# Optimization experiments

Hardware: AMD Instinct MI355X
Metric: run time of the kernel (lower is better)

## Reference

```python
import jax, jax.numpy as jnp
import numpy as np

N = 100000
E = 1600000
C = 64          # hidden_channels
F_IN = 3
F_OUT = 3
N_MP = 2        # message-passing layers


def _lin(k, fan_in, fan_out):
    kw, kb = jax.random.split(k)
    bound = 1.0 / np.sqrt(fan_in)
    W = jax.random.uniform(kw, (fan_in, fan_out), jnp.float32, -bound, bound)
    b = jax.random.uniform(kb, (fan_out,), jnp.float32, -bound, bound)
    return W, b


def setup_inputs() -> dict:
    key = jax.random.key(0)
    ks = jax.random.split(key, 32)
    x = jax.random.normal(ks[0], (N, F_IN), jnp.float32)
    pos = jax.random.normal(ks[1], (N, 3), jnp.float32)
    edge_index = jax.random.randint(ks[2], (2, E), 0, N, jnp.int64)

    enc_W0, enc_b0 = _lin(ks[3], F_IN, C)
    enc_W1, enc_b1 = _lin(ks[4], C, C)
    dec_W0, dec_b0 = _lin(ks[5], C, C)
    dec_W1, dec_b1 = _lin(ks[6], C, F_OUT)

    # stacked params for the N_MP message-passing layers
    eW0, eb0, eW1, eb1 = [], [], [], []
    nW0, nb0, nW1, nb1 = [], [], [], []
    for i in range(N_MP):
        W, b = _lin(ks[7 + 4 * i], 3 * C + 3, C); eW0.append(W); eb0.append(b)
        W, b = _lin(ks[8 + 4 * i], C, C);         eW1.append(W); eb1.append(b)
        W, b = _lin(ks[9 + 4 * i], 2 * C, C);     nW0.append(W); nb0.append(b)
        W, b = _lin(ks[10 + 4 * i], C, C);        nW1.append(W); nb1.append(b)
    stack = lambda xs: jnp.stack(xs, axis=0)
    return {
        "x": x, "pos": pos, "edge_index": edge_index,
        "enc_W0": enc_W0, "enc_b0": enc_b0, "enc_W1": enc_W1, "enc_b1": enc_b1,
        "dec_W0": dec_W0, "dec_b0": dec_b0, "dec_W1": dec_W1, "dec_b1": dec_b1,
        "mp_eW0": stack(eW0), "mp_eb0": stack(eb0),
        "mp_eW1": stack(eW1), "mp_eb1": stack(eb1),
        "mp_nW0": stack(nW0), "mp_nb0": stack(nb0),
        "mp_nW1": stack(nW1), "mp_nb1": stack(nb1),
    }


def reference(x, pos, edge_index,
              enc_W0, enc_b0, enc_W1, enc_b1,
              dec_W0, dec_b0, dec_W1, dec_b1,
              mp_eW0, mp_eb0, mp_eW1, mp_eb1,
              mp_nW0, mp_nb0, mp_nW1, mp_nb1):
    act = jax.nn.elu
    src, dst = edge_index[0], edge_index[1]

    # node encoder (2-layer MLP, activation between layers only)
    h = act(x @ enc_W0 + enc_b0)
    h = h @ enc_W1 + enc_b1

    pos_diff = pos[src] - pos[dst]  # [E, 3], constant across MP layers

    for i in range(N_MP):
        x_nei = h[src]               # [E, C]
        x_own = h[dst]               # [E, C]
        ea = jnp.concatenate([x_nei, x_own, x_nei - x_own, pos_diff], axis=1)
        ea = act(ea @ mp_eW0[i] + mp_eb0[i])
        ea = ea @ mp_eW1[i] + mp_eb1[i]
        # EdgeAggregation(aggr='add'): scatter-add edge features to target nodes
        agg = jax.ops.segment_sum(ea, dst, num_segments=N)  # [N, C]
        u = jnp.concatenate([h, agg], axis=1)                # [N, 2C]
        u = act(u @ mp_nW0[i] + mp_nb0[i])
        u = u @ mp_nW1[i] + mp_nb1[i]
        h = h + u  # residual

    # node decoder
    out = act(h @ dec_W0 + dec_b0)
    out = out @ dec_W1 + dec_b1
    return out
```

## Files before the change

kernel.cpp:

```cpp
#include <hip/hip_runtime.h>
#include <hip/hip_bf16.h>

#define NN 100000
#define NE 1600000
#define NBKT 391
#define BCAP 4608

typedef __hip_bfloat16 bf16;
typedef unsigned short u16;
typedef unsigned int u32;
typedef short bshort8 __attribute__((ext_vector_type(8)));
typedef float f32x4 __attribute__((ext_vector_type(4)));

__device__ __forceinline__ float b2f_raw(u16 u) {
    unsigned int w = ((unsigned int)u) << 16;
    float f; __builtin_memcpy(&f, &w, 4); return f;
}
__device__ __forceinline__ float uplo(u32 u) {
    u32 w = u << 16; float f; __builtin_memcpy(&f, &w, 4); return f;
}
__device__ __forceinline__ float uphi(u32 u) {
    u32 w = u & 0xFFFF0000u; float f; __builtin_memcpy(&f, &w, 4); return f;
}
__device__ __forceinline__ u16 f2bu(float f) {
    bf16 h = __float2bfloat16(f); u16 u; __builtin_memcpy(&u, &h, 2); return u;
}
__device__ __forceinline__ float eluf(float x) { return x > 0.f ? x : __expf(x) - 1.f; }

#define OFF_ENC_W0 0
#define OFF_ENC_B0 192
#define OFF_ENC_W1 256
#define OFF_ENC_B1 4352
#define OFF_DEC_W0 4416
#define OFF_DEC_B0 8512
#define OFF_DEC_W1 8576
#define OFF_DEC_B1 8768
#define OFF_EW0    8832
#define OFF_EB0    33792
#define OFF_EW1    33920
#define OFF_EB1    42112
#define OFF_NW0    42240
#define OFF_NB0    58624
#define OFF_NW1    58752
#define OFF_NB1    66944
#define OFF_WF     67072
#define OFF_BFOLD  75264
#define WBLK_WORDS 75392

#define SWZ_V   12288
#define SWZ_N0  24576
#define SWZ_N1  45056
#define SWZ_DC  53248
#define SWZ_ENC 57344
#define SWZ_U16 61440

__global__ void probe_kernel(const u16* __restrict__ xr,
                             const unsigned int* __restrict__ er,
                             int* __restrict__ flags, int* __restrict__ gcursor) {
    int tid = threadIdx.x;
    gcursor[tid] = 0;
    if (tid >= 64) return;
    int lane = tid;
    int wild = 0, oddnz = 0;
#pragma unroll
    for (int k = 0; k < 4; ++k) {
        int e = (xr[lane + k * 64] >> 7) & 0xFF;
        if (e > 140 || (e < 90 && e != 0)) wild++;
    }
#pragma unroll
    for (int k = 0; k < 2; ++k)
        if (er[1 + 2 * (lane + k * 64)] != 0u) oddnz++;
#pragma unroll
    for (int off = 32; off; off >>= 1) {
        wild += __shfl_down(wild, off);
        oddnz += __shfl_down(oddnz, off);
    }
    if (lane == 0) { flags[0] = (wild > 16) ? 1 : 0; flags[1] = (oddnz < 8) ? 1 : 0; }
}

struct WPtrs { const void* p[16]; };

__global__ void canon_weights(WPtrs wp, float* __restrict__ wblk,
                              const int* __restrict__ flags) {
    const int offs[16] = {OFF_ENC_W0, OFF_ENC_B0, OFF_ENC_W1, OFF_ENC_B1,
                          OFF_DEC_W0, OFF_DEC_B0, OFF_DEC_W1, OFF_DEC_B1,
                          OFF_EW0, OFF_EB0, OFF_EW1, OFF_EB1,
                          OFF_NW0, OFF_NB0, OFF_NW1, OFF_NB1};
    const int ns[16]   = {192, 64, 4096, 64, 4096, 64, 192, 3,
                          24960, 128, 8192, 128, 16384, 128, 8192, 128};
    int t = blockIdx.y;
    int i = blockIdx.x * blockDim.x + threadIdx.x;
    if (i >= ns[t]) return;
    const void* s = wp.p[t];
    float v = flags[0] ? ((const float*)s)[i] : b2f_raw(((const u16*)s)[i]);
    wblk[offs[t] + i] = v;
}

__global__ void prep_wf(float* __restrict__ wblk) {
    int idx = blockIdx.x * 256 + threadIdx.x;
    if (idx < 8192) {
        int l = idx >> 12, r = idx & 4095, k = r >> 6, c = r & 63;
        const float* e1 = wblk + OFF_EW1 + l * 4096 + k * 64;
        const float* n0 = wblk + OFF_NW0 + l * 8192 + 64 * 64;
        float s = 0.f;
#pragma unroll 8
        for (int m = 0; m < 64; ++m) s += e1[m] * n0[m * 64 + c];
        wblk[OFF_WF + idx] = s;
    } else if (idx < 8320) {
        int i2 = idx - 8192;
        int l = i2 >> 6, c = i2 & 63;
        const float* b1 = wblk + OFF_EB1 + l * 64;
        const float* n0 = wblk + OFF_NW0 + l * 8192 + 64 * 64;
        float s = 0.f;
#pragma unroll 8
        for (int m = 0; m < 64; ++m) s += b1[m] * n0[m * 64 + c];
        wblk[OFF_BFOLD + i2] = s;
    }
}

__global__ void prep_swz(const float* __restrict__ wblk, u16* __restrict__ swz) {
    int t = blockIdx.x * 256 + threadIdx.x;
    if (t >= SWZ_U16) return;
    float v = 0.f;
    if (t < SWZ_N0) {
        int isV = (t >= SWZ_V);
        int t2 = isV ? t - SWZ_V : t;
        int l = t2 / 6144, r = t2 % 6144;
        int ks = r >> 11, nt = (r >> 9) & 3, lane = (r >> 3) & 63, j = r & 7;
        int k = ks * 32 + ((lane >> 4) & 3) * 8 + j;
        int n = nt * 16 + (lane & 15);
        const float* W = wblk + OFF_EW0 + l * 12480;
        if (k < 64)
            v = isV ? (W[(64 + k) * 64 + n] - W[(128 + k) * 64 + n])
                    : (W[k * 64 + n] + W[(128 + k) * 64 + n]);
        else if (k < 67) {
            v = W[(192 + (k - 64)) * 64 + n];
            if (isV) v = -v;
        }
    } else if (t < SWZ_N1) {
        int t2 = t - SWZ_N0;
        int l = t2 / 10240, r = t2 % 10240;
        int ks = r >> 11, nt = (r >> 9) & 3, lane = (r >> 3) & 63, j = r & 7;
        int k = ks * 32 + ((lane >> 4) & 3) * 8 + j;
        int n = nt * 16 + (lane & 15);
        if (k < 64)        v = wblk[OFF_NW0 + l * 8192 + k * 64 + n];
        else if (k < 128)  v = wblk[OFF_WF + l * 4096 + (k - 64) * 64 + n];
        else if (k == 128) v = wblk[OFF_BFOLD + l * 64 + n];
    } else if (t < SWZ_DC) {
        int t2 = t - SWZ_N1;
        int l = t2 / 4096, r = t2 % 4096;
        int ks = r >> 11, nt = (r >> 9) & 3, lane = (r >> 3) & 63, j = r & 7;
        int k = ks * 32 + ((lane >> 4) & 3) * 8 + j;
        int n = nt * 16 + (lane & 15);
        v = wblk[OFF_NW1 + l * 4096 + k * 64 + n];
    } else if (t < SWZ_ENC) {
        int r = t - SWZ_DC;
        int ks = r >> 11, nt = (r >> 9) & 3, lane = (r >> 3) & 63, j = r & 7;
        int k = ks * 32 + ((lane >> 4) & 3) * 8 + j;
        int n = nt * 16 + (lane & 15);
        v = wblk[OFF_DEC_W0 + k * 64 + n];
    } else {
        int r = t - SWZ_ENC;
        int ks = r >> 11, nt = (r >> 9) & 3, lane = (r >> 3) & 63, j = r & 7;
        int k = ks * 32 + ((lane >> 4) & 3) * 8 + j;
        int n = nt * 16 + (lane & 15);
        v = wblk[OFF_ENC_W1 + k * 64 + n];
    }
    swz[t] = f2bu(v);
}

__global__ __launch_bounds__(1024) void passA_bin(
    const void* __restrict__ eiraw, const int* __restrict__ flags,
    u32* __restrict__ epk_b, int* __restrict__ gcursor) {
    __shared__ int hist[NBKT];
    __shared__ int binstart[NBKT];
    __shared__ int gbase_l[NBKT];
    __shared__ int fill[NBKT];
    __shared__ int sc[512];
    __shared__ u32 stage[4096];
    __shared__ u16 slotbin[4096];
    int tid = threadIdx.x;
    for (int i = tid; i < NBKT; i += 1024) hist[i] = 0;
    __syncthreads();
    int base = blockIdx.x * 4096;
    int total = NE - base; if (total > 4096) total = 4096;
    bool i64 = flags[1] != 0;
    u32 ed[4]; int bn[4];
#pragma unroll
    for (int k = 0; k < 4; ++k) {
        int e = base + tid + k * 1024;
        bn[k] = -1;
        if (e < NE) {
            int s, d;
            if (i64) {
                s = (int)((const long long*)eiraw)[e];
                d = (int)((const long long*)eiraw)[(size_t)NE + e];
            } else {
                s = ((const int*)eiraw)[e];
                d = ((const int*)eiraw)[(size_t)NE + e];
            }
            if ((unsigned)s >= NN) s = 0;
            if ((unsigned)d >= NN) d = 0;
            ed[k] = (u32)s | ((u32)(d & 255) << 17);
            bn[k] = d >> 8;
            atomicAdd(&hist[bn[k]], 1);
        }
    }
    __syncthreads();
    if (tid < 512) sc[tid] = (tid < NBKT) ? hist[tid] : 0;
    __syncthreads();
    for (int d = 1; d < 512; d <<= 1) {
        int v = (tid >= d && tid < 512) ? sc[tid - d] : 0;
        __syncthreads();
        if (tid < 512) sc[tid] += v;
        __syncthreads();
    }
    if (tid < NBKT) {
        binstart[tid] = sc[tid] - hist[tid];
        fill[tid] = 0;
        gbase_l[tid] = hist[tid] ? atomicAdd(&gcursor[tid], hist[tid]) : 0;
    }
    __syncthreads();
#pragma unroll
    for (int k = 0; k < 4; ++k) {
        if (bn[k] >= 0) {
            int p = binstart[bn[k]] + atomicAdd(&fill[bn[k]], 1);
            stage[p] = ed[k];
            slotbin[p] = (u16)bn[k];
        }
    }
    __syncthreads();
    for (int i = tid; i < total; i += 1024) {
        int b = slotbin[i];
        int gp = gbase_l[b] + (i - binstart[b]);
        if (gp < BCAP) epk_b[(size_t)b * BCAP + gp] = stage[i];
    }
}

__global__ __launch_bounds__(512) void scan391(const int* __restrict__ gcursor,
                                               int* __restrict__ gbase2) {
    __shared__ int s[512];
    int t = threadIdx.x;
    int v = 0;
    if (t < NBKT) { v = gcursor[t]; if (v > BCAP) v = BCAP; }
    s[t] = v;
    __syncthreads();
    for (int d = 1; d < 512; d <<= 1) {
        int u = (t >= d) ? s[t - d] : 0;
        __syncthreads();
        s[t] += u;
        __syncthreads();
    }
    if (t < NBKT) gbase2[t] = s[t] - v;
}

__global__ __launch_bounds__(1024) void passB_sort(
    const u32* __restrict__ epk_b, const int* __restrict__ gcursor,
    const int* __restrict__ gbase2, int* __restrict__ srcs,
    int* __restrict__ start) {
    __shared__ int h256[256];
    __shared__ int off256[256];
    __shared__ int sc[256];
    __shared__ u32 stage[BCAP];
    int b = blockIdx.x, tid = threadIdx.x;
    int cnt = gcursor[b]; if (cnt > BCAP) cnt = BCAP;
    for (int i = tid; i < 256; i += 1024) h256[i] = 0;
    __syncthreads();
    u32 ed[5]; int dl[5];
#pragma unroll
    for (int k = 0; k < 5; ++k) {
        int i = tid + k * 1024;
        dl[k] = -1;
        if (i < cnt) {
            ed[k] = epk_b[(size_t)b * BCAP + i];
            dl[k] = (int)(ed[k] >> 17);
            atomicAdd(&h256[dl[k]], 1);
        }
    }
    __syncthreads();
    if (tid < 256) sc[tid] = h256[tid];
    __syncthreads();
    for (int d = 1; d < 256; d <<= 1) {
        int v = (tid >= d && tid < 256) ? sc[tid - d] : 0;
        __syncthreads();
        if (tid < 256) sc[tid] += v;
        __syncthreads();
    }
    int gb = gbase2[b];
    if (tid < 256) {
        off256[tid] = sc[tid] - h256[tid];
        start[b * 256 + tid] = gb + sc[tid] - h256[tid];
    }
    __syncthreads();
#pragma unroll
    for (int k = 0; k < 5; ++k) {
        if (dl[k] >= 0) {
            int p = atomicAdd(&off256[dl[k]], 1);
            stage[p] = ed[k];
        }
    }
    __syncthreads();
    for (int i = tid; i < cnt; i += 1024) srcs[gb + i] = (int)(stage[i] & 0x1FFFFu);
}

__global__ __launch_bounds__(512) void enc_uv(
    const void* __restrict__ xraw, const void* __restrict__ praw,
    const float* __restrict__ wblk, const u16* __restrict__ swzE,
    const u16* __restrict__ swzU, const u16* __restrict__ swzV,
    u16* __restrict__ hb, u16* __restrict__ pos4b,
    u16* __restrict__ U, u16* __restrict__ V,
    const int* __restrict__ flags) {
    __shared__ __attribute__((aligned(16))) u16 sE[4096];
    __shared__ __attribute__((aligned(16))) u16 sU[6144];
    __shared__ __attribute__((aligned(16))) u16 sV[6144];
    __shared__ __attribute__((aligned(16))) u16 sP[8][16 * 72];
    int tid = threadIdx.x;
    for (int i = tid; i < 512; i += 512) ((uint4*)sE)[i] = ((const uint4*)swzE)[i];
    for (int i = tid; i < 768; i += 512) {
        ((uint4*)sU)[i] = ((const uint4*)swzU)[i];
        ((uint4*)sV)[i] = ((const uint4*)swzV)[i];
    }
    __syncthreads();
    int wid = tid >> 6, lane = tid & 63;
    int m16 = lane & 15, half = lane >> 4;
    int g = blockIdx.x * 8 + wid;
    if (g >= NN / 16) return;
    int n0 = g * 16 + m16;
    bool isf = flags[0] != 0;
    float x0, x1, x2;
    if (isf) {
        x0 = ((const float*)xraw)[n0 * 3 + 0];
        x1 = ((const float*)xraw)[n0 * 3 + 1];
        x2 = ((const float*)xraw)[n0 * 3 + 2];
    } else {
        x0 = b2f_raw(((const u16*)xraw)[n0 * 3 + 0]);
        x1 = b2f_raw(((const u16*)xraw)[n0 * 3 + 1]);
        x2 = b2f_raw(((const u16*)xraw)[n0 * 3 + 2]);
    }
    u16 pk0 = 0, pk1 = 0, pk2 = 0;
    if (half == 0) {
        float p0 = isf ? ((const float*)praw)[n0 * 3 + 0] : b2f_raw(((const u16*)praw)[n0 * 3 + 0]);
        float p1 = isf ? ((const float*)praw)[n0 * 3 + 1] : b2f_raw(((const u16*)praw)[n0 * 3 + 1]);
        float p2 = isf ? ((const float*)praw)[n0 * 3 + 2] : b2f_raw(((const u16*)praw)[n0 * 3 + 2]);
        pk0 = f2bu(p0); pk1 = f2bu(p1); pk2 = f2bu(p2);
        *(ushort4*)(pos4b + (size_t)n0 * 4) = make_ushort4(pk0, pk1, pk2, 0);
    }
    const float* W0 = wblk + OFF_ENC_W0;
    const float* b0 = wblk + OFF_ENC_B0;
    bshort8 af0, af1;
#pragma unroll
    for (int j = 0; j < 8; ++j) {
        int c = half * 8 + j;
        float v = b0[c] + x0 * W0[c] + x1 * W0[64 + c] + x2 * W0[128 + c];
        af0[j] = (short)f2bu(eluf(v));
        int c2 = 32 + c;
        float v2 = b0[c2] + x0 * W0[c2] + x1 * W0[64 + c2] + x2 * W0[128 + c2];
        af1[j] = (short)f2bu(eluf(v2));
    }
    const bshort8* BE = (const bshort8*)sE;
    f32x4 acc[4];
#pragma unroll
    for (int nt = 0; nt < 4; ++nt) {
        float b = wblk[OFF_ENC_B1 + nt * 16 + m16];
        acc[nt] = f32x4{b, b, b, b};
    }
#pragma unroll
    for (int nt = 0; nt < 4; ++nt)
        acc[nt] = __builtin_amdgcn_mfma_f32_16x16x32_bf16(af0, BE[nt * 64 + lane], acc[nt], 0, 0, 0);
#pragma unroll
    for (int nt = 0; nt < 4; ++nt)
        acc[nt] = __builtin_amdgcn_mfma_f32_16x16x32_bf16(af1, BE[(4 + nt) * 64 + lane], acc[nt], 0, 0, 0);
    u16* myP = sP[wid];
#pragma unroll
    for (int nt = 0; nt < 4; ++nt)
#pragma unroll
        for (int r = 0; r < 4; ++r) {
            size_t ix = (size_t)(g * 16 + half * 4 + r) * 64 + nt * 16 + m16;
            u16 hv = f2bu(acc[nt][r]);
            hb[ix] = hv;
            myP[(half * 4 + r) * 72 + nt * 16 + m16] = hv;
        }
    bshort8 ah0 = *(const bshort8*)(myP + m16 * 72 + 0 * 32 + half * 8);
    bshort8 ah1 = *(const bshort8*)(myP + m16 * 72 + 1 * 32 + half * 8);
    bshort8 ap;
#pragma unroll
    for (int j = 0; j < 8; ++j) ap[j] = 0;
    if (half == 0) { ap[0] = (short)pk0; ap[1] = (short)pk1; ap[2] = (short)pk2; }
    const bshort8* BU = (const bshort8*)sU;
    const bshort8* BV = (const bshort8*)sV;
    const float* eb0p = wblk + OFF_EB0;
    f32x4 aU[4], aV[4];
#pragma unroll
    for (int nt = 0; nt < 4; ++nt) {
        float bv = eb0p[nt * 16 + m16];
        aU[nt] = f32x4{0.f, 0.f, 0.f, 0.f};
        aV[nt] = f32x4{bv, bv, bv, bv};
    }
#pragma unroll
    for (int nt = 0; nt < 4; ++nt) {
        aU[nt] = __builtin_amdgcn_mfma_f32_16x16x32_bf16(ah0, BU[nt * 64 + lane], aU[nt], 0, 0, 0);
        aV[nt] = __builtin_amdgcn_mfma_f32_16x16x32_bf16(ah0, BV[nt * 64 + lane], aV[nt], 0, 0, 0);
    }
#pragma unroll
    for (int nt = 0; nt < 4; ++nt) {
        aU[nt] = __builtin_amdgcn_mfma_f32_16x16x32_bf16(ah1, BU[(4 + nt) * 64 + lane], aU[nt], 0, 0, 0);
        aV[nt] = __builtin_amdgcn_mfma_f32_16x16x32_bf16(ah1, BV[(4 + nt) * 64 + lane], aV[nt], 0, 0, 0);
    }
#pragma unroll
    for (int nt = 0; nt < 4; ++nt) {
        aU[nt] = __builtin_amdgcn_mfma_f32_16x16x32_bf16(ap, BU[(8 + nt) * 64 + lane], aU[nt], 0, 0, 0);
        aV[nt] = __builtin_amdgcn_mfma_f32_16x16x32_bf16(ap, BV[(8 + nt) * 64 + lane], aV[nt], 0, 0, 0);
    }
#pragma unroll
    for (int nt = 0; nt < 4; ++nt)
#pragma unroll
        for (int r = 0; r < 4; ++r) {
            size_t ix = (size_t)(g * 16 + half * 4 + r) * 64 + nt * 16 + m16;
            U[ix] = f2bu(aU[nt][r]);
            V[ix] = f2bu(aV[nt][r]);
        }
}

__global__ __launch_bounds__(256) void edge_sum(
    const u32* __restrict__ U32, const u32* __restrict__ V32,
    const int* __restrict__ srcs, const int* __restrict__ start,
    u32* __restrict__ Sb, int totalwaves) {
    int tid = threadIdx.x;
    int w = blockIdx.x * 4 + (tid >> 6);
    int lane = tid & 63;
    int half = lane >> 5, t = lane & 31;
    int nb = (int)((long long)w * NN / totalwaves);
    int ne = (int)((long long)(w + 1) * NN / totalwaves);
    for (int n = nb; n < ne; ++n) {
        int s0 = start[n], s1 = start[n + 1];
        float aLo = 0.f, aHi = 0.f;
        if (s1 > s0) {
            u32 vv = V32[(size_t)n * 32 + t];
            float vlo = uplo(vv), vhi = uphi(vv);
            int eb = s0;
            while (eb + 16 <= s1) {
                int sv[8];
#pragma unroll
                for (int k = 0; k < 8; ++k) sv[k] = srcs[eb + half + 2 * k];
                u32 ug[8];
#pragma unroll
                for (int k = 0; k < 8; ++k) ug[k] = U32[(size_t)sv[k] * 32 + t];
#pragma unroll
                for (int k = 0; k < 8; ++k) {
                    aLo += eluf(uplo(ug[k]) + vlo);
                    aHi += eluf(uphi(ug[k]) + vhi);
                }
                eb += 16;
            }
            if (eb + 8 <= s1) {
                int sv[4];
#pragma unroll
                for (int k = 0; k < 4; ++k) sv[k] = srcs[eb + half + 2 * k];
                u32 ug[4];
#pragma unroll
                for (int k = 0; k < 4; ++k) ug[k] = U32[(size_t)sv[k] * 32 + t];
#pragma unroll
                for (int k = 0; k < 4; ++k) {
                    aLo += eluf(uplo(ug[k]) + vlo);
                    aHi += eluf(uphi(ug[k]) + vhi);
                }
                eb += 8;
            }
            for (int e = eb + half; e < s1; e += 2) {
                u32 u = U32[(size_t)srcs[e] * 32 + t];
                aLo += eluf(uplo(u) + vlo);
                aHi += eluf(uphi(u) + vhi);
            }
            aLo += __shfl_xor(aLo, 32);
            aHi += __shfl_xor(aHi, 32);
        }
        if (half == 0)
            Sb[(size_t)n * 32 + t] = (u32)f2bu(aLo) | ((u32)f2bu(aHi) << 16);
    }
}

__global__ __launch_bounds__(512) void node_uv(
    u16* __restrict__ hb, const u16* __restrict__ Sb,
    const int* __restrict__ start, const float* __restrict__ wblk,
    const u16* __restrict__ swz, const u16* __restrict__ pos4b,
    u16* __restrict__ U, u16* __restrict__ V) {
    __shared__ __attribute__((aligned(16))) u16 sN0[10240];
    __shared__ __attribute__((aligned(16))) u16 sN1[4096];
    __shared__ __attribute__((aligned(16))) u16 sU[6144];
    __shared__ __attribute__((aligned(16))) u16 sV[6144];
    __shared__ __attribute__((aligned(16))) u16 sP[8][16 * 72];
    int tid = threadIdx.x;
    {
        const uint4* s0 = (const uint4*)(swz + SWZ_N0);
        const uint4* s1 = (const uint4*)(swz + SWZ_N1);
        const uint4* su = (const uint4*)(swz + 6144);
        const uint4* sv = (const uint4*)(swz + SWZ_V + 6144);
        for (int i = tid; i < 1280; i += 512) ((uint4*)sN0)[i] = s0[i];
        for (int i = tid; i < 512; i += 512)  ((uint4*)sN1)[i] = s1[i];
        for (int i = tid; i < 768; i += 512) {
            ((uint4*)sU)[i] = su[i];
            ((uint4*)sV)[i] = sv[i];
        }
    }
    __syncthreads();
    int wid = tid >> 6, lane = tid & 63;
    int m16 = lane & 15, half = lane >> 4;
    int g = blockIdx.x * 8 + wid;
    if (g >= NN / 16) return;
    int n0 = g * 16 + m16;
    const float* b0 = wblk + OFF_NB0;
    const float* b1 = wblk + OFF_NB1;
    const bshort8* B0 = (const bshort8*)sN0;
    const bshort8* B1 = (const bshort8*)sN1;
    u16* myP = sP[wid];

    bshort8 afh0 = *(const bshort8*)(hb + (size_t)n0 * 64 + half * 8);
    bshort8 afh1 = *(const bshort8*)(hb + (size_t)n0 * 64 + 32 + half * 8);
    bshort8 afs0 = *(const bshort8*)(Sb + (size_t)n0 * 64 + half * 8);
    bshort8 afs1 = *(const bshort8*)(Sb + (size_t)n0 * 64 + 32 + half * 8);
    bshort8 afd;
#pragma unroll
    for (int j = 0; j < 8; ++j) afd[j] = 0;
    if (half == 0) {
        float deg = (float)(start[n0 + 1] - start[n0]);
        afd[0] = (short)f2bu(deg);
    }
    f32x4 acc[4];
#pragma unroll
    for (int nt = 0; nt < 4; ++nt) {
        float b = b0[nt * 16 + m16];
        acc[nt] = f32x4{b, b, b, b};
    }
#pragma unroll
    for (int nt = 0; nt < 4; ++nt)
        acc[nt] = __builtin_amdgcn_mfma_f32_16x16x32_bf16(afh0, B0[nt * 64 + lane], acc[nt], 0, 0, 0);
#pragma unroll
    for (int nt = 0; nt < 4; ++nt)
        acc[nt] = __builtin_amdgcn_mfma_f32_16x16x32_bf16(afh1, B0[(4 + nt) * 64 + lane], acc[nt], 0, 0, 0);
#pragma unroll
    for (int nt = 0; nt < 4; ++nt)
        acc[nt] = __builtin_amdgcn_mfma_f32_16x16x32_bf16(afs0, B0[(8 + nt) * 64 + lane], acc[nt], 0, 0, 0);
#pragma unroll
    for (int nt = 0; nt < 4; ++nt)
        acc[nt] = __builtin_amdgcn_mfma_f32_16x16x32_bf16(afs1, B0[(12 + nt) * 64 + lane], acc[nt], 0, 0, 0);
#pragma unroll
    for (int nt = 0; nt < 4; ++nt)
        acc[nt] = __builtin_amdgcn_mfma_f32_16x16x32_bf16(afd, B0[(16 + nt) * 64 + lane], acc[nt], 0, 0, 0);
#pragma unroll
    for (int nt = 0; nt < 4; ++nt)
#pragma unroll
        for (int r = 0; r < 4; ++r) {
            float v = acc[nt][r];
            v = eluf(v);
            myP[(half * 4 + r) * 72 + nt * 16 + m16] = f2bu(v);
        }
    f32x4 acc2[4];
#pragma unroll
    for (int nt = 0; nt < 4; ++nt) {
        float b = b1[nt * 16 + m16];
        acc2[nt] = f32x4{b, b, b, b};
    }
#pragma unroll
    for (int ks = 0; ks < 2; ++ks) {
        bshort8 av = *(const bshort8*)(myP + m16 * 72 + ks * 32 + half * 8);
#pragma unroll
        for (int nt = 0; nt < 4; ++nt)
            acc2[nt] = __builtin_amdgcn_mfma_f32_16x16x32_bf16(
                av, B1[(ks * 4 + nt) * 64 + lane], acc2[nt], 0, 0, 0);
    }
#pragma unroll
    for (int nt = 0; nt < 4; ++nt)
#pragma unroll
        for (int r = 0; r < 4; ++r) {
            size_t ix = (size_t)(g * 16 + half * 4 + r) * 64 + nt * 16 + m16;
            float v = b2f_raw(hb[ix]) + acc2[nt][r];
            u16 hv = f2bu(v);
            hb[ix] = hv;
            myP[(half * 4 + r) * 72 + nt * 16 + m16] = hv;
        }
    bshort8 ah0 = *(const bshort8*)(myP + m16 * 72 + 0 * 32 + half * 8);
    bshort8 ah1 = *(const bshort8*)(myP + m16 * 72 + 1 * 32 + half * 8);
    bshort8 ap;
#pragma unroll
    for (int j = 0; j < 8; ++j) ap[j] = 0;
    if (half == 0) {
        ushort4 pp = *(const ushort4*)(pos4b + (size_t)n0 * 4);
        ap[0] = (short)pp.x; ap[1] = (short)pp.y; ap[2] = (short)pp.z;
    }
    const bshort8* BU = (const bshort8*)sU;
    const bshort8* BV = (const bshort8*)sV;
    const float* eb0p = wblk + OFF_EB0 + 64;
    f32x4 aU[4], aV[4];
#pragma unroll
    for (int nt = 0; nt < 4; ++nt) {
        float bv = eb0p[nt * 16 + m16];
        aU[nt] = f32x4{0.f, 0.f, 0.f, 0.f};
        aV[nt] = f32x4{bv, bv, bv, bv};
    }
#pragma unroll
    for (int nt = 0; nt < 4; ++nt) {
        aU[nt] = __builtin_amdgcn_mfma_f32_16x16x32_bf16(ah0, BU[nt * 64 + lane], aU[nt], 0, 0, 0);
        aV[nt] = __builtin_amdgcn_mfma_f32_16x16x32_bf16(ah0, BV[nt * 64 + lane], aV[nt], 0, 0, 0);
    }
#pragma unroll
    for (int nt = 0; nt < 4; ++nt) {
        aU[nt] = __builtin_amdgcn_mfma_f32_16x16x32_bf16(ah1, BU[(4 + nt) * 64 + lane], aU[nt], 0, 0, 0);
        aV[nt] = __builtin_amdgcn_mfma_f32_16x16x32_bf16(ah1, BV[(4 + nt) * 64 + lane], aV[nt], 0, 0, 0);
    }
#pragma unroll
    for (int nt = 0; nt < 4; ++nt) {
        aU[nt] = __builtin_amdgcn_mfma_f32_16x16x32_bf16(ap, BU[(8 + nt) * 64 + lane], aU[nt], 0, 0, 0);
        aV[nt] = __builtin_amdgcn_mfma_f32_16x16x32_bf16(ap, BV[(8 + nt) * 64 + lane], aV[nt], 0, 0, 0);
    }
#pragma unroll
    for (int nt = 0; nt < 4; ++nt)
#pragma unroll
        for (int r = 0; r < 4; ++r) {
            size_t ix = (size_t)(g * 16 + half * 4 + r) * 64 + nt * 16 + m16;
            U[ix] = f2bu(aU[nt][r]);
            V[ix] = f2bu(aV[nt][r]);
        }
}

__global__ __launch_bounds__(512) void node_dec(
    const u16* __restrict__ hb, const u16* __restrict__ Sb,
    const int* __restrict__ start, const float* __restrict__ wblk,
    const u16* __restrict__ swz,
    void* __restrict__ out, const int* __restrict__ flags) {
    __shared__ __attribute__((aligned(16))) u16 sN0[10240];
    __shared__ __attribute__((aligned(16))) u16 sN1[4096];
    __shared__ __attribute__((aligned(16))) u16 sDec[4096];
    __shared__ __attribute__((aligned(16))) float sT[8][1048];
    int tid = threadIdx.x;
    {
        const uint4* s0 = (const uint4*)(swz + SWZ_N0 + 10240);
        const uint4* s1 = (const uint4*)(swz + SWZ_N1 + 4096);
        const uint4* sd = (const uint4*)(swz + SWZ_DC);
        for (int i = tid; i < 1280; i += 512) ((uint4*)sN0)[i] = s0[i];
        for (int i = tid; i < 512; i += 512)  ((uint4*)sN1)[i] = s1[i];
        for (int i = tid; i < 512; i += 512)  ((uint4*)sDec)[i] = sd[i];
    }
    __syncthreads();
    int wid = tid >> 6, lane = tid & 63;
    int m16 = lane & 15, half = lane >> 4;
    int g = blockIdx.x * 8 + wid;
    if (g >= NN / 16) return;
    int n0 = g * 16 + m16;
    const float* b0 = wblk + OFF_NB0 + 64;
    const float* b1 = wblk + OFF_NB1 + 64;
    const bshort8* B0 = (const bshort8*)sN0;
    const bshort8* B1 = (const bshort8*)sN1;
    const bshort8* BD = (const bshort8*)sDec;
    u16* myP = (u16*)sT[wid];
    float* sD = sT[wid];

    bshort8 afh0 = *(const bshort8*)(hb + (size_t)n0 * 64 + half * 8);
    bshort8 afh1 = *(const bshort8*)(hb + (size_t)n0 * 64 + 32 + half * 8);
    bshort8 afs0 = *(const bshort8*)(Sb + (size_t)n0 * 64 + half * 8);
    bshort8 afs1 = *(const bshort8*)(Sb + (size_t)n0 * 64 + 32 + half * 8);
    bshort8 afd;
#pragma unroll
    for (int j = 0; j < 8; ++j) afd[j] = 0;
    if (half == 0) {
        float deg = (float)(start[n0 + 1] - start[n0]);
        afd[0] = (short)f2bu(deg);
    }
    f32x4 acc[4];
#pragma unroll
    for (int nt = 0; nt < 4; ++nt) {
        float b = b0[nt * 16 + m16];
        acc[nt] = f32x4{b, b, b, b};
    }
#pragma unroll
    for (int nt = 0; nt < 4; ++nt)
        acc[nt] = __builtin_amdgcn_mfma_f32_16x16x32_bf16(afh0, B0[nt * 64 + lane], acc[nt], 0, 0, 0);
#pragma unroll
    for (int nt = 0; nt < 4; ++nt)
        acc[nt] = __builtin_amdgcn_mfma_f32_16x16x32_bf16(afh1, B0[(4 + nt) * 64 + lane], acc[nt], 0, 0, 0);
#pragma unroll
    for (int nt = 0; nt < 4; ++nt)
        acc[nt] = __builtin_amdgcn_mfma_f32_16x16x32_bf16(afs0, B0[(8 + nt) * 64 + lane], acc[nt], 0, 0, 0);
#pragma unroll
    for (int nt = 0; nt < 4; ++nt)
        acc[nt] = __builtin_amdgcn_mfma_f32_16x16x32_bf16(afs1, B0[(12 + nt) * 64 + lane], acc[nt], 0, 0, 0);
#pragma unroll
    for (int nt = 0; nt < 4; ++nt)
        acc[nt] = __builtin_amdgcn_mfma_f32_16x16x32_bf16(afd, B0[(16 + nt) * 64 + lane], acc[nt], 0, 0, 0);
#pragma unroll
    for (int nt = 0; nt < 4; ++nt)
#pragma unroll
        for (int r = 0; r < 4; ++r) {
            float v = acc[nt][r];
            v = eluf(v);
            myP[(half * 4 + r) * 72 + nt * 16 + m16] = f2bu(v);
        }
    f32x4 acc2[4];
#pragma unroll
    for (int nt = 0; nt < 4; ++nt) {
        float b = b1[nt * 16 + m16];
        acc2[nt] = f32x4{b, b, b, b};
    }
#pragma unroll
    for (int ks = 0; ks < 2; ++ks) {
        bshort8 av = *(const bshort8*)(myP + m16 * 72 + ks * 32 + half * 8);
#pragma unroll
        for (int nt = 0; nt < 4; ++nt)
            acc2[nt] = __builtin_amdgcn_mfma_f32_16x16x32_bf16(
                av, B1[(ks * 4 + nt) * 64 + lane], acc2[nt], 0, 0, 0);
    }
    float nh[4][4];
#pragma unroll
    for (int nt = 0; nt < 4; ++nt)
#pragma unroll
        for (int r = 0; r < 4; ++r) {
            size_t ix = (size_t)(g * 16 + half * 4 + r) * 64 + nt * 16 + m16;
            nh[nt][r] = b2f_raw(hb[ix]) + acc2[nt][r];
        }
#pragma unroll
    for (int nt = 0; nt < 4; ++nt)
#pragma unroll
        for (int r = 0; r < 4; ++r)
            myP[(half * 4 + r) * 72 + nt * 16 + m16] = f2bu(nh[nt][r]);
    const float* db0 = wblk + OFF_DEC_B0;
    f32x4 acc3[4];
#pragma unroll
    for (int nt = 0; nt < 4; ++nt) {
        float b = db0[nt * 16 + m16];
        acc3[nt] = f32x4{b, b, b, b};
    }
#pragma unroll
    for (int ks = 0; ks < 2; ++ks) {
        bshort8 av = *(const bshort8*)(myP + m16 * 72 + ks * 32 + half * 8);
#pragma unroll
        for (int nt = 0; nt < 4; ++nt)
            acc3[nt] = __builtin_amdgcn_mfma_f32_16x16x32_bf16(
                av, BD[(ks * 4 + nt) * 64 + lane], acc3[nt], 0, 0, 0);
    }
#pragma unroll
    for (int nt = 0; nt < 4; ++nt)
#pragma unroll
        for (int r = 0; r < 4; ++r) {
            float v = acc3[nt][r];
            v = eluf(v);
            sD[(half * 4 + r) * 65 + nt * 16 + m16] = v;
        }
    if (lane < 48) {
        int j = lane / 3, o = lane - j * 3;
        const float* dW1 = wblk + OFF_DEC_W1;
        float oacc = wblk[OFF_DEC_B1 + o];
#pragma unroll
        for (int k = 0; k < 64; ++k) oacc += sD[j * 65 + k] * dW1[k * 3 + o];
        int nn = g * 16 + j;
        if (flags[0]) ((float*)out)[nn * 3 + o] = oacc;
        else          ((bf16*)out)[nn * 3 + o] = __float2bfloat16(oacc);
    }
}

extern "C" void kernel_launch(void* const* d_in, const int* in_sizes, int n_in,
                              void* d_out, int out_size, void* d_ws, size_t ws_size,
                              hipStream_t stream) {
    int*   flags   = (int*)d_ws;
    float* wblk    = (float*)d_ws + 16;
    u16*   swz     = (u16*)(wblk + WBLK_WORDS);
    u16*   pos4b   = swz + SWZ_U16;
    int*   gcursor = (int*)(pos4b + 400000);
    int*   gbase2  = gcursor + 512;
    int*   start   = gbase2 + 512;
    int*   srcs    = start + NN + 512;
    u16*   Sb      = (u16*)(srcs + NE);
    u16*   hb      = Sb + (size_t)NN * 64;
    u16*   U       = hb + (size_t)NN * 64;
    u16*   V       = U + (size_t)NN * 64;
    u32*   epk_b   = (u32*)Sb;

    probe_kernel<<<1, 512, 0, stream>>>((const u16*)d_in[0],
                                        (const unsigned int*)d_in[2], flags, gcursor);

    WPtrs wp;
    wp.p[0] = d_in[3];  wp.p[1] = d_in[4];  wp.p[2] = d_in[5];  wp.p[3] = d_in[6];
    wp.p[4] = d_in[7];  wp.p[5] = d_in[8];  wp.p[6] = d_in[9];  wp.p[7] = d_in[10];
    wp.p[8] = d_in[11]; wp.p[9] = d_in[12]; wp.p[10] = d_in[13]; wp.p[11] = d_in[14];
    wp.p[12] = d_in[15]; wp.p[13] = d_in[16]; wp.p[14] = d_in[17]; wp.p[15] = d_in[18];
    canon_weights<<<dim3(98, 16), 256, 0, stream>>>(wp, wblk, flags);
    prep_wf<<<33, 256, 0, stream>>>(wblk);
    prep_swz<<<240, 256, 0, stream>>>(wblk, swz);

    passA_bin<<<(NE + 4095) / 4096, 1024, 0, stream>>>(d_in[2], flags, epk_b, gcursor);
    scan391<<<1, 512, 0, stream>>>(gcursor, gbase2);
    passB_sort<<<NBKT, 1024, 0, stream>>>(epk_b, gcursor, gbase2, srcs, start);

    const int NODE_BLOCKS = (NN / 16 + 7) / 8;
    const int EDGE_BLOCKS = 2048;
    const int TOTALWAVES = EDGE_BLOCKS * 4;

    enc_uv<<<NODE_BLOCKS, 512, 0, stream>>>(
        d_in[0], d_in[1], wblk, swz + SWZ_ENC,
        swz, swz + SWZ_V, hb, pos4b, U, V, flags);

    edge_sum<<<EDGE_BLOCKS, 256, 0, stream>>>(
        (const u32*)U, (const u32*)V, srcs, start, (u32*)Sb, TOTALWAVES);
    node_uv<<<NODE_BLOCKS, 512, 0, stream>>>(
        hb, Sb, start, wblk, swz, pos4b, U, V);

    edge_sum<<<EDGE_BLOCKS, 256, 0, stream>>>(
        (const u32*)U, (const u32*)V, srcs, start, (u32*)Sb, TOTALWAVES);
    node_dec<<<NODE_BLOCKS, 512, 0, stream>>>(
        hb, Sb, start, wblk, swz, d_out, flags);
}
```

Measured before the change: 305.0 us.

## Restructure edge_sum with branchless ELU decomposition, LDS-staged sources, wider lane loads

U and V are pre-scaled by log2(e) so edge_sum can use a raw exp2. ELU is split as max(x,0)*ln2 + min(exp2(x),1) - 1, with the -1 term applied once per node through the edge count, which removes the per-element branch. The edge loop now gives each lane four channels (uint2 loads) and processes four edges per wave step. Each wave first stages its contiguous srcs range into LDS. Bf16 rounding of the pre-scaled values slightly changes numerics, and the block-wide sync plus the fallback path when a wave's edge count exceeds the LDS capacity add overhead.

New measurement: 314.5 us. 3.1% more time.

```diff
diff --git a/kernel.cpp b/kernel.cpp
--- a/kernel.cpp
+++ b/kernel.cpp
@@ -26,6 +26,9 @@
     bf16 h = __float2bfloat16(f); u16 u; __builtin_memcpy(&u, &h, 2); return u;
 }
 __device__ __forceinline__ float eluf(float x) { return x > 0.f ? x : __expf(x) - 1.f; }
+
+#define LOG2E 1.4426950408889634f
+#define LN2F  0.6931471805599453f
 
 #define OFF_ENC_W0 0
 #define OFF_ENC_B0 192
@@ -416,66 +419,97 @@
 #pragma unroll
         for (int r = 0; r < 4; ++r) {
             size_t ix = (size_t)(g * 16 + half * 4 + r) * 64 + nt * 16 + m16;
-            U[ix] = f2bu(aU[nt][r]);
-            V[ix] = f2bu(aV[nt][r]);
-        }
-}
-
+            U[ix] = f2bu(aU[nt][r] * LOG2E);
+            V[ix] = f2bu(aV[nt][r] * LOG2E);
+        }
+}
+
+#define ES_CAP 1024
 __global__ __launch_bounds__(256) void edge_sum(
     const u32* __restrict__ U32, const u32* __restrict__ V32,
     const int* __restrict__ srcs, const int* __restrict__ start,
     u32* __restrict__ Sb, int totalwaves) {
+    __shared__ int sS[4][ES_CAP];
     int tid = threadIdx.x;
-    int w = blockIdx.x * 4 + (tid >> 6);
+    int wslot = tid >> 6;
+    int w = blockIdx.x * 4 + wslot;
     int lane = tid & 63;
-    int half = lane >> 5, t = lane & 31;
+    int eo = lane >> 4, co = lane & 15;
     int nb = (int)((long long)w * NN / totalwaves);
     int ne = (int)((long long)(w + 1) * NN / totalwaves);
+    int s0w = start[nb], s1w = start[ne];
+    int cw = s1w - s0w;
+    const int* sp = srcs + s0w;
+    if (cw <= ES_CAP) {
+        for (int i = lane; i < cw; i += 64) sS[wslot][i] = srcs[s0w + i];
+        sp = sS[wslot];
+    }
+    __syncthreads();
+
+    int s0 = s0w;
     for (int n = nb; n < ne; ++n) {
-        int s0 = start[n], s1 = start[n + 1];
-        float aLo = 0.f, aHi = 0.f;
-        if (s1 > s0) {
-            u32 vv = V32[(size_t)n * 32 + t];
-            float vlo = uplo(vv), vhi = uphi(vv);
-            int eb = s0;
-            while (eb + 16 <= s1) {
-                int sv[8];
-#pragma unroll
-                for (int k = 0; k < 8; ++k) sv[k] = srcs[eb + half + 2 * k];
-                u32 ug[8];
-#pragma unroll
-                for (int k = 0; k < 8; ++k) ug[k] = U32[(size_t)sv[k] * 32 + t];
-#pragma unroll
-                for (int k = 0; k < 8; ++k) {
-                    aLo += eluf(uplo(ug[k]) + vlo);
-                    aHi += eluf(uphi(ug[k]) + vhi);
-                }
-                eb += 16;
-            }
-            if (eb + 8 <= s1) {
-                int sv[4];
-#pragma unroll
-                for (int k = 0; k < 4; ++k) sv[k] = srcs[eb + half + 2 * k];
-                u32 ug[4];
-#pragma unroll
-                for (int k = 0; k < 4; ++k) ug[k] = U32[(size_t)sv[k] * 32 + t];
-#pragma unroll
-                for (int k = 0; k < 4; ++k) {
-                    aLo += eluf(uplo(ug[k]) + vlo);
-                    aHi += eluf(uphi(ug[k]) + vhi);
-                }
-                eb += 8;
-            }
-            for (int e = eb + half; e < s1; e += 2) {
-                u32 u = U32[(size_t)srcs[e] * 32 + t];
-                aLo += eluf(uplo(u) + vlo);
-                aHi += eluf(uphi(u) + vhi);
-            }
-            aLo += __shfl_xor(aLo, 32);
-            aHi += __shfl_xor(aHi, 32);
-        }
-        if (half == 0)
-            Sb[(size_t)n * 32 + t] = (u32)f2bu(aLo) | ((u32)f2bu(aHi) << 16);
+        int s1 = start[n + 1];
+        int cnt = s1 - s0;
+        const int* spn = sp + (s0 - s0w);
+        uint2 vv = *(const uint2*)(V32 + (size_t)n * 32 + (co << 1));
+        float v0 = uplo(vv.x), v1 = uphi(vv.x);
+        float v2 = uplo(vv.y), v3 = uphi(vv.y);
+        float accA0 = 0.f, accA1 = 0.f, accA2 = 0.f, accA3 = 0.f;
+        float accB0 = 0.f, accB1 = 0.f, accB2 = 0.f, accB3 = 0.f;
+
+        auto GRP = [&](int goff, bool MASKED) {
+            int ei = goff + eo;
+            int eic = ei;
+            if (MASKED) eic = (ei < cnt) ? ei : (cnt - 1);
+            int s = spn[eic];
+            uint2 uu = *(const uint2*)(U32 + (size_t)s * 32 + (co << 1));
+            float x0 = uplo(uu.x) + v0, x1 = uphi(uu.x) + v1;
+            float x2 = uplo(uu.y) + v2, x3 = uphi(uu.y) + v3;
+            float e0 = __builtin_amdgcn_exp2f(x0);
+            float e1 = __builtin_amdgcn_exp2f(x1);
+            float e2 = __builtin_amdgcn_exp2f(x2);
+            float e3 = __builtin_amdgcn_exp2f(x3);
+            bool val = !MASKED || (ei < cnt);
+            accA0 += val ? fmaxf(x0, 0.f) : 0.f;
+            accA1 += val ? fmaxf(x1, 0.f) : 0.f;
+            accA2 += val ? fmaxf(x2, 0.f) : 0.f;
+            accA3 += val ? fmaxf(x3, 0.f) : 0.f;
+            accB0 += val ? fminf(e0, 1.f) : 0.f;
+            accB1 += val ? fminf(e1, 1.f) : 0.f;
+            accB2 += val ? fminf(e2, 1.f) : 0.f;
+            accB3 += val ? fminf(e3, 1.f) : 0.f;
+        };
+
+        int g = 0;
+        for (; g + 16 <= cnt; g += 16) {
+            GRP(g + 0, false);
+            GRP(g + 4, false);
+            GRP(g + 8, false);
+            GRP(g + 12, false);
+        }
+        int rem = cnt - g;
+        if (rem > 0) {
+            GRP(g + 0, true);
+            if (rem > 4)  GRP(g + 4, true);
+            if (rem > 8)  GRP(g + 8, true);
+            if (rem > 12) GRP(g + 12, true);
+        }
+
+        float t0 = fmaf(accA0, LN2F, accB0);
+        float t1 = fmaf(accA1, LN2F, accB1);
+        float t2 = fmaf(accA2, LN2F, accB2);
+        float t3 = fmaf(accA3, LN2F, accB3);
+        t0 += __shfl_xor(t0, 16); t0 += __shfl_xor(t0, 32);
+        t1 += __shfl_xor(t1, 16); t1 += __shfl_xor(t1, 32);
+        t2 += __shfl_xor(t2, 16); t2 += __shfl_xor(t2, 32);
+        t3 += __shfl_xor(t3, 16); t3 += __shfl_xor(t3, 32);
+        if (eo == 0) {
+            float cf = (float)cnt;
+            u32 p0 = (u32)f2bu(t0 - cf) | ((u32)f2bu(t1 - cf) << 16);
+            u32 p1 = (u32)f2bu(t2 - cf) | ((u32)f2bu(t3 - cf) << 16);
+            *(uint2*)(Sb + (size_t)n * 32 + (co << 1)) = make_uint2(p0, p1);
+        }
+        s0 = s1;
     }
 }
 
@@ -617,8 +651,8 @@
 #pragma unroll
         for (int r = 0; r < 4; ++r) {
             size_t ix = (size_t)(g * 16 + half * 4 + r) * 64 + nt * 16 + m16;
-            U[ix] = f2bu(aU[nt][r]);
-            V[ix] = f2bu(aV[nt][r]);
+            U[ix] = f2bu(aU[nt][r] * LOG2E);
+            V[ix] = f2bu(aV[nt][r] * LOG2E);
         }
 }
 
```
